# Kernel tuning notes

Measured on AMD Instinct MI355X. Metric: run time of the kernel, lower is better.

Reference implementation:

```python
import jax, jax.numpy as jnp
import numpy as np
from jax import lax

S = 2                      # window half-size (matches init_kwargs s)
K = 2 * S + 1              # kernel size = 5
SZ = float(K ** 3)         # number of voxels in the window
EPS = 1e-10


def _box_sum(x):
    """Replicate-pad then valid 3D box-sum with an all-ones K^3 kernel.
    x: [N, 1, D, H, W] -> [N, 1, D, H, W]. Same math as F.pad(mode='replicate')
    followed by Conv3d(ones kernel, valid)."""
    xp = jnp.pad(x, ((0, 0), (0, 0), (S, S), (S, S), (S, S)), mode='edge')
    kern = jnp.ones((1, 1, K, K, K), dtype=x.dtype)
    return lax.conv_general_dilated(
        xp, kern, window_strides=(1, 1, 1), padding='VALID',
        dimension_numbers=('NCDHW', 'OIDHW', 'NCDHW'))


def setup_inputs() -> dict:
    key = jax.random.key(0)
    k1, k2 = jax.random.split(key)
    shape = (2, 1, 160, 160, 160)
    im_fixed = jax.random.normal(k1, shape, dtype=jnp.float32)
    im_moving = jax.random.normal(k2, shape, dtype=jnp.float32)
    mask = jnp.ones(shape, dtype=jnp.float32)
    return {"im_fixed": im_fixed, "im_moving": im_moving, "mask": mask}


def reference(im_fixed, im_moving, mask):
    # local means
    u_F = _box_sum(im_fixed) / SZ
    u_M = _box_sum(im_moving) / SZ
    # local variances (box-sum of squared centered values, then / SZ)
    sigma_F = jnp.sqrt(_box_sum((im_fixed - u_F) ** 2) / SZ)
    sigma_M = jnp.sqrt(_box_sum((im_moving - u_M) ** 2) / SZ)
    # normalized images
    n_F = (im_fixed - u_F) / (sigma_F + EPS)
    n_M = (im_moving - u_M) / (sigma_M + EPS)
    # local cross-correlation map (box-sum, NOT divided by SZ, as in torch code)
    cross = _box_sum(n_F * n_M)
    # reduce: negative masked sum of squared LCC
    return -1.0 * jnp.sum(cross ** 2 * mask)
```

## Files before the change

### kernel.cpp

```cpp
#include <hip/hip_runtime.h>

namespace {

constexpr int LEN   = 160;
constexpr int PLANE = LEN * LEN;
constexpr int VOL   = LEN * PLANE;
constexpr float INV_SZ = 1.0f / 125.0f;
constexpr float EPS_   = 1e-10f;

constexpr int BLK = 512;

constexpr int FTX = 32, FTY = 16, FZC = 32;
constexpr int FRX = FTX + 4, FRY = FTY + 4;
constexpr int FNRAW = FRX * FRY;
constexpr int FNBX = 5, FNBY = 10, FNXY = 50, FNCHZ = 5;

constexpr int STX = 32, STY = 32, SZC = 16;
constexpr int SRX = STX + 4, SRY = STY + 4;
constexpr int SNRAW = SRX * SRY;
constexpr int SNBX = 5, SNBY = 5, SNXY = 25, SNCHZ = 10;

constexpr int NWG = 500, QW = 62, RW = 4;

__device__ __forceinline__ int clampi(int v) {
  return v < 0 ? 0 : (v > LEN - 1 ? LEN - 1 : v);
}

__device__ __forceinline__ int swz(int g) {
  const int xcd = g & 7, idx = g >> 3;
  return (xcd < RW) ? xcd * (QW + 1) + idx
                    : RW * (QW + 1) + (xcd - RW) * QW + idx;
}

__global__ __launch_bounds__(BLK) void fuseAB(const float* __restrict__ inA,
                                              const float* __restrict__ inB,
                                              float* __restrict__ outP) {
  __shared__ __align__(16) float raw[2][2][FRY][FRX];
  __shared__ __align__(16) float xs [4][2][FRY][FTX];

  const int tid = threadIdx.x;
  const int g = blockIdx.x + FNBX * (blockIdx.y + FNBY * blockIdx.z);
  const int w = swz(g);
  const int batch = w / 250, rem = w % 250;
  const int zc = rem / FNXY, tl = rem % FNXY;
  const int x0 = (tl % FNBX) * FTX;
  const int y0 = (tl / FNBX) * FTY;
  const int z0 = zc * FZC;
  const size_t base = (size_t)batch * VOL;

  int off[2]; float* ldst[2][2][2];
  bool act[2];
#pragma unroll
  for (int j = 0; j < 2; ++j) {
    int i = tid + j * BLK;
    act[j] = i < FNRAW;
    int ii = act[j] ? i : 0;
    const int ry = ii / FRX, rx = ii % FRX;
    off[j] = clampi(y0 - 2 + ry) * LEN + clampi(x0 - 2 + rx);
#pragma unroll
    for (int f = 0; f < 2; ++f)
#pragma unroll
      for (int p = 0; p < 2; ++p) ldst[j][f][p] = &raw[f][p][ry][rx];
  }

  const float* tsrc[2]; float* tdst[2];
#pragma unroll
  for (int k = 0; k < 2; ++k) {
    int tt = (k == 0) ? tid : tid + BLK;
    if (tt >= 640) tt = 0;
    const int p = tt / 320, r1 = tt % 320;
    const int f = r1 / 160, r2 = r1 % 160;
    const int r = r2 / 8,  c = r2 % 8;
    tsrc[k] = &raw[f][p][r][4 * c];
    tdst[k] = &xs[f][p][r][4 * c];
  }

  const bool qact = tid < 256;
  const int ly  = tid >> 4;
  const int lx0 = (tid & 15) * 2;
  const int sOff = (y0 + ly) * LEN + (x0 + lx0);

  float pA[2][2], pB[2][2];
  float2 rzF[6], rzM[6], rzF2[6], rzM2[6];
  float2 cnF[4], cnM[4];

  auto loadPair = [&](int t) {
#pragma unroll
    for (int p = 0; p < 2; ++p) {
      const size_t pb = base + (size_t)clampi(t + p) * PLANE;
#pragma unroll
      for (int j = 0; j < 2; ++j)
        if (act[j]) { pA[p][j] = inA[pb + off[j]]; pB[p][j] = inB[pb + off[j]]; }
    }
  };
  auto depositPair = [&]() {
#pragma unroll
    for (int p = 0; p < 2; ++p)
#pragma unroll
      for (int j = 0; j < 2; ++j)
        if (act[j]) { *ldst[j][0][p] = pA[p][j]; *ldst[j][1][p] = pB[p][j]; }
  };

  auto xsumTask = [&](int k) {
    const float4 u = *(const float4*)tsrc[k];
    const float4 v = *(const float4*)(tsrc[k] + 4);
    const float m = u.y + u.z + u.w;
    float4 s;
    s.x = m + u.x + v.x;
    s.y = m + v.x + v.y;
    s.z = s.y - u.y + v.z;
    s.w = s.z - u.z + v.w;
    *(float4*)tdst[k] = s;
    float4 uq, vq;
    uq.x = u.x * u.x; uq.y = u.y * u.y; uq.z = u.z * u.z; uq.w = u.w * u.w;
    vq.x = v.x * v.x; vq.y = v.y * v.y; vq.z = v.z * v.z; vq.w = v.w * v.w;
    const float mq = uq.y + uq.z + uq.w;
    float4 q;
    q.x = mq + uq.x + vq.x;
    q.y = mq + vq.x + vq.y;
    q.z = q.y - uq.y + vq.z;
    q.w = q.z - uq.z + vq.w;
    *(float4*)(tdst[k] + 2 * 2 * FRY * FTX) = q;
  };

  loadPair(z0 - 2);
  depositPair();
  __syncthreads();

  for (int t = z0 - 2; t <= z0 + FZC; t += 2) {
    if (t + 2 <= z0 + FZC) loadPair(t + 2);

    xsumTask(0);
    if (tid < 128) xsumTask(1);

    if (qact) {
      cnF[0] = cnF[2]; cnF[1] = cnF[3]; cnM[0] = cnM[2]; cnM[1] = cnM[3];
      cnF[2] = *(const float2*)&raw[0][0][ly + 2][lx0 + 2];
      cnF[3] = *(const float2*)&raw[0][1][ly + 2][lx0 + 2];
      cnM[2] = *(const float2*)&raw[1][0][ly + 2][lx0 + 2];
      cnM[3] = *(const float2*)&raw[1][1][ly + 2][lx0 + 2];
    }

    __syncthreads();

    if (t + 2 <= z0 + FZC) depositPair();

    if (qact) {
#pragma unroll
      for (int s = 0; s < 4; ++s) {
        rzF[s] = rzF[s + 2]; rzM[s] = rzM[s + 2];
        rzF2[s] = rzF2[s + 2]; rzM2[s] = rzM2[s + 2];
      }
#pragma unroll
      for (int p = 0; p < 2; ++p) {
        float2 sf = {0.f, 0.f}, sm = {0.f, 0.f};
        float2 sf2 = {0.f, 0.f}, sm2 = {0.f, 0.f};
#pragma unroll
        for (int k = 0; k < 5; ++k) {
          const float2 a  = *(const float2*)&xs[0][p][ly + k][lx0];
          const float2 b  = *(const float2*)&xs[1][p][ly + k][lx0];
          const float2 a2 = *(const float2*)&xs[2][p][ly + k][lx0];
          const float2 b2 = *(const float2*)&xs[3][p][ly + k][lx0];
          sf.x += a.x;   sf.y += a.y;   sm.x += b.x;   sm.y += b.y;
          sf2.x += a2.x; sf2.y += a2.y; sm2.x += b2.x; sm2.y += b2.y;
        }
        rzF[4 + p] = sf; rzM[4 + p] = sm;
        rzF2[4 + p] = sf2; rzM2[4 + p] = sm2;
      }

      if (t >= z0 + 2) {
#pragma unroll
        for (int q = 0; q < 2; ++q) {
          const int zo = t - 2 + q;
          float2 bF = {0.f, 0.f}, bM = {0.f, 0.f};
          float2 bF2 = {0.f, 0.f}, bM2 = {0.f, 0.f};
#pragma unroll
          for (int s = 0; s < 5; ++s) {
            bF.x += rzF[q + s].x;   bF.y += rzF[q + s].y;
            bM.x += rzM[q + s].x;   bM.y += rzM[q + s].y;
            bF2.x += rzF2[q + s].x; bF2.y += rzF2[q + s].y;
            bM2.x += rzM2[q + s].x; bM2.y += rzM2[q + s].y;
          }
          float2 o;
          {
            const float uF = bF.x * INV_SZ, uM = bM.x * INV_SZ;
            const float vF = fmaxf(bF2.x * INV_SZ - uF * uF, 0.f);
            const float vM = fmaxf(bM2.x * INV_SZ - uM * uM, 0.f);
            o.x = ((cnF[q].x - uF) * (cnM[q].x - uM)) /
                  ((sqrtf(vF) + EPS_) * (sqrtf(vM) + EPS_));
          }
          {
            const float uF = bF.y * INV_SZ, uM = bM.y * INV_SZ;
            const float vF = fmaxf(bF2.y * INV_SZ - uF * uF, 0.f);
            const float vM = fmaxf(bM2.y * INV_SZ - uM * uM, 0.f);
            o.y = ((cnF[q].y - uF) * (cnM[q].y - uM)) /
                  ((sqrtf(vF) + EPS_) * (sqrtf(vM) + EPS_));
          }
          *(float2*)&outP[base + (size_t)zo * PLANE + sOff] = o;
        }
      }
    }
    __syncthreads();
  }
}

__global__ __launch_bounds__(BLK) void slab1_reduce(const float* __restrict__ p,
                                                    const float* __restrict__ mask,
                                                    float* __restrict__ out) {
  __shared__ __align__(16) float raw[2][SRY][SRX];
  __shared__ __align__(16) float xs [2][SRY][SRX];
  __shared__ float wsum[BLK / 64];

  const int tid = threadIdx.x;
  const int g = blockIdx.x + SNBX * (blockIdx.y + SNBY * blockIdx.z);
  const int w = swz(g);
  const int batch = w / 250, rem = w % 250;
  const int zc = rem / SNXY, tl = rem % SNXY;
  const int x0 = (tl % SNBX) * STX;
  const int y0 = (tl / SNBX) * STY;
  const int z0 = zc * SZC;
  const size_t base = (size_t)batch * VOL;

  int off[3], lly[3], llx[3];
  bool act[3];
#pragma unroll
  for (int j = 0; j < 3; ++j) {
    int i = tid + j * BLK;
    act[j] = i < SNRAW;
    int ii = act[j] ? i : 0;
    lly[j] = ii / SRX; llx[j] = ii % SRX;
    off[j] = clampi(y0 - 2 + lly[j]) * LEN + clampi(x0 - 2 + llx[j]);
  }
  const int ly  = tid >> 4;
  const int lx0 = (tid & 15) * 2;

  float pf[2][3];
  float2 rz[6];
  float acc = 0.f;

  auto loadPair = [&](int t) {
#pragma unroll
    for (int pp = 0; pp < 2; ++pp) {
      const size_t pb = base + (size_t)clampi(t + pp) * PLANE;
#pragma unroll
      for (int j = 0; j < 3; ++j)
        if (act[j]) pf[pp][j] = p[pb + off[j]];
    }
  };
  auto depositPair = [&]() {
#pragma unroll
    for (int pp = 0; pp < 2; ++pp)
#pragma unroll
      for (int j = 0; j < 3; ++j)
        if (act[j]) raw[pp][lly[j]][llx[j]] = pf[pp][j];
  };

  loadPair(z0 - 2);
  depositPair();
  __syncthreads();

  for (int t = z0 - 2; t <= z0 + SZC; t += 2) {
    if (t + 2 <= z0 + SZC) loadPair(t + 2);

    if (tid < 288) {
      const int c = tid & 7, r = tid >> 3;
#pragma unroll
      for (int pp = 0; pp < 2; ++pp) {
        const float* rp = &raw[pp][r][4 * c];
        const float4 u = *(const float4*)rp;
        const float4 v = *(const float4*)(rp + 4);
        const float m = u.y + u.z + u.w;
        float4 s;
        s.x = m + u.x + v.x;
        s.y = m + v.x + v.y;
        s.z = s.y - u.y + v.z;
        s.w = s.z - u.z + v.w;
        *(float4*)&xs[pp][r][4 * c] = s;
      }
    }
    __syncthreads();

    if (t + 2 <= z0 + SZC) depositPair();

#pragma unroll
    for (int s = 0; s < 4; ++s) rz[s] = rz[s + 2];
#pragma unroll
    for (int pp = 0; pp < 2; ++pp) {
      float2 s2 = {0.f, 0.f};
#pragma unroll
      for (int k = 0; k < 5; ++k) {
        const float2 a = *(const float2*)&xs[pp][ly + k][lx0];
        s2.x += a.x; s2.y += a.y;
      }
      rz[4 + pp] = s2;
    }

    if (t >= z0 + 2) {
#pragma unroll
      for (int q = 0; q < 2; ++q) {
        const int zo = t - 2 + q;
        float2 bs = {0.f, 0.f};
#pragma unroll
        for (int s = 0; s < 5; ++s) { bs.x += rz[q + s].x; bs.y += rz[q + s].y; }
        const size_t gg = base + (size_t)zo * PLANE + (size_t)(y0 + ly) * LEN + (x0 + lx0);
        const float2 mk = *(const float2*)&mask[gg];
        acc += bs.x * bs.x * mk.x + bs.y * bs.y * mk.y;
      }
    }
    __syncthreads();
  }

#pragma unroll
  for (int o = 32; o > 0; o >>= 1) acc += __shfl_down(acc, o, 64);
  const int lane = tid & 63, wid = tid >> 6;
  if (lane == 0) wsum[wid] = acc;
  __syncthreads();
  if (tid == 0) {
    float tt = 0.f;
#pragma unroll
    for (int ww = 0; ww < BLK / 64; ++ww) tt += wsum[ww];
    atomicAdd(out, -tt);
  }
}

}

extern "C" void kernel_launch(void* const* d_in, const int* in_sizes, int n_in,
                              void* d_out, int out_size, void* d_ws, size_t ws_size,
                              hipStream_t stream) {
  const float* F    = (const float*)d_in[0];
  const float* M    = (const float*)d_in[1];
  const float* mask = (const float*)d_in[2];
  float* out = (float*)d_out;

  float* pB = (float*)d_ws;

  hipMemsetAsync(d_out, 0, sizeof(float), stream);

  dim3 gf(FNBX, FNBY, FNCHZ * 2), blk(BLK);
  dim3 gs(SNBX, SNBY, SNCHZ * 2);

  fuseAB<<<gf, blk, 0, stream>>>(F, M, pB);
  slab1_reduce<<<gs, blk, 0, stream>>>(pB, mask, out);
}
```

Before: 163.3 us.

## Double-buffer LDS slabs and deepen global prefetch in both stencil kernels

Both kernels now keep two LDS copies of the raw and x-summed slabs and alternate between them. Each z-step needs one barrier instead of two, and global loads are issued two steps ahead into a second register set. The aim is to hide barrier and global-load latency on the streaming z-loop. In exchange LDS use per block roughly doubles, to about 63 KB in fuseAB, and register pressure rises, which may lower the number of resident blocks.

Result: no change. 162.8 us (-0.3%).

```diff
diff --git a/kernel.cpp b/kernel.cpp
--- a/kernel.cpp
+++ b/kernel.cpp
@@ -20,7 +20,7 @@
 constexpr int SNRAW = SRX * SRY;
 constexpr int SNBX = 5, SNBY = 5, SNXY = 25, SNCHZ = 10;
 
-constexpr int NWG = 500, QW = 62, RW = 4;
+constexpr int QW = 62, RW = 4;
 
 __device__ __forceinline__ int clampi(int v) {
   return v < 0 ? 0 : (v > LEN - 1 ? LEN - 1 : v);
@@ -35,8 +35,12 @@
 __global__ __launch_bounds__(BLK) void fuseAB(const float* __restrict__ inA,
                                               const float* __restrict__ inB,
                                               float* __restrict__ outP) {
-  __shared__ __align__(16) float raw[2][2][FRY][FRX];
-  __shared__ __align__(16) float xs [4][2][FRY][FTX];
+  __shared__ __align__(16) float raw[2][2][2][FRY][FRX];
+  __shared__ __align__(16) float xs [2][4][2][FRY][FTX];
+  constexpr int RAWB = 2 * 2 * FRY * FRX;
+  constexpr int XSB  = 4 * 2 * FRY * FTX;
+  constexpr int AS   = 2 * FRY * FTX;
+  constexpr int PS   = FRY * FTX;
 
   const int tid = threadIdx.x;
   const int g = blockIdx.x + FNBX * (blockIdx.y + FNBY * blockIdx.z);
@@ -48,7 +52,7 @@
   const int z0 = zc * FZC;
   const size_t base = (size_t)batch * VOL;
 
-  int off[2]; float* ldst[2][2][2];
+  int off[2]; float* ld0[2][2][2];
   bool act[2];
 #pragma unroll
   for (int j = 0; j < 2; ++j) {
@@ -60,10 +64,10 @@
 #pragma unroll
     for (int f = 0; f < 2; ++f)
 #pragma unroll
-      for (int p = 0; p < 2; ++p) ldst[j][f][p] = &raw[f][p][ry][rx];
-  }
-
-  const float* tsrc[2]; float* tdst[2];
+      for (int p = 0; p < 2; ++p) ld0[j][f][p] = &raw[0][f][p][ry][rx];
+  }
+
+  const float* ts0[2]; float* td0[2];
 #pragma unroll
   for (int k = 0; k < 2; ++k) {
     int tt = (k == 0) ? tid : tid + BLK;
@@ -71,46 +75,52 @@
     const int p = tt / 320, r1 = tt % 320;
     const int f = r1 / 160, r2 = r1 % 160;
     const int r = r2 / 8,  c = r2 % 8;
-    tsrc[k] = &raw[f][p][r][4 * c];
-    tdst[k] = &xs[f][p][r][4 * c];
+    ts0[k] = &raw[0][f][p][r][4 * c];
+    td0[k] = &xs[0][f][p][r][4 * c];
   }
 
   const bool qact = tid < 256;
   const int ly  = tid >> 4;
   const int lx0 = (tid & 15) * 2;
   const int sOff = (y0 + ly) * LEN + (x0 + lx0);
-
-  float pA[2][2], pB[2][2];
+  const float* yb0 = &xs[0][0][0][ly][lx0];
+
+  float s0A[2][2], s0B[2][2], s1A[2][2], s1B[2][2];
   float2 rzF[6], rzM[6], rzF2[6], rzM2[6];
   float2 cnF[4], cnM[4];
 
-  auto loadPair = [&](int t) {
+  auto loadPair = [&](int t, float (&ra)[2][2], float (&rb)[2][2]) {
 #pragma unroll
     for (int p = 0; p < 2; ++p) {
       const size_t pb = base + (size_t)clampi(t + p) * PLANE;
 #pragma unroll
       for (int j = 0; j < 2; ++j)
-        if (act[j]) { pA[p][j] = inA[pb + off[j]]; pB[p][j] = inB[pb + off[j]]; }
-    }
-  };
-  auto depositPair = [&]() {
+        if (act[j]) { ra[p][j] = inA[pb + off[j]]; rb[p][j] = inB[pb + off[j]]; }
+    }
+  };
+  auto depositPair = [&](int buf, float (&ra)[2][2], float (&rb)[2][2]) {
 #pragma unroll
     for (int p = 0; p < 2; ++p)
 #pragma unroll
       for (int j = 0; j < 2; ++j)
-        if (act[j]) { *ldst[j][0][p] = pA[p][j]; *ldst[j][1][p] = pB[p][j]; }
-  };
-
-  auto xsumTask = [&](int k) {
-    const float4 u = *(const float4*)tsrc[k];
-    const float4 v = *(const float4*)(tsrc[k] + 4);
+        if (act[j]) {
+          ld0[j][0][p][buf * RAWB] = ra[p][j];
+          ld0[j][1][p][buf * RAWB] = rb[p][j];
+        }
+  };
+
+  auto xsumTask = [&](int buf, int k) {
+    const float* src = ts0[k] + buf * RAWB;
+    float* dst = td0[k] + buf * XSB;
+    const float4 u = *(const float4*)src;
+    const float4 v = *(const float4*)(src + 4);
     const float m = u.y + u.z + u.w;
     float4 s;
     s.x = m + u.x + v.x;
     s.y = m + v.x + v.y;
     s.z = s.y - u.y + v.z;
     s.w = s.z - u.z + v.w;
-    *(float4*)tdst[k] = s;
+    *(float4*)dst = s;
     float4 uq, vq;
     uq.x = u.x * u.x; uq.y = u.y * u.y; uq.z = u.z * u.z; uq.w = u.w * u.w;
     vq.x = v.x * v.x; vq.y = v.y * v.y; vq.z = v.z * v.z; vq.w = v.w * v.w;
@@ -120,30 +130,27 @@
     q.y = mq + vq.x + vq.y;
     q.z = q.y - uq.y + vq.z;
     q.w = q.z - uq.z + vq.w;
-    *(float4*)(tdst[k] + 2 * 2 * FRY * FTX) = q;
-  };
-
-  loadPair(z0 - 2);
-  depositPair();
-  __syncthreads();
-
-  for (int t = z0 - 2; t <= z0 + FZC; t += 2) {
-    if (t + 2 <= z0 + FZC) loadPair(t + 2);
-
-    xsumTask(0);
-    if (tid < 128) xsumTask(1);
+    *(float4*)(dst + 2 * AS) = q;
+  };
+
+  auto body = [&](int buf, int t,
+                  float (&dA)[2][2], float (&dB)[2][2],
+                  float (&lA)[2][2], float (&lB)[2][2]) {
+    if (t + 2 <= z0 + FZC) depositPair(buf ^ 1, dA, dB);
+    if (t + 4 <= z0 + FZC) loadPair(t + 4, lA, lB);
+
+    xsumTask(buf, 0);
+    if (tid < 128) xsumTask(buf, 1);
 
     if (qact) {
       cnF[0] = cnF[2]; cnF[1] = cnF[3]; cnM[0] = cnM[2]; cnM[1] = cnM[3];
-      cnF[2] = *(const float2*)&raw[0][0][ly + 2][lx0 + 2];
-      cnF[3] = *(const float2*)&raw[0][1][ly + 2][lx0 + 2];
-      cnM[2] = *(const float2*)&raw[1][0][ly + 2][lx0 + 2];
-      cnM[3] = *(const float2*)&raw[1][1][ly + 2][lx0 + 2];
+      cnF[2] = *(const float2*)&raw[buf][0][0][ly + 2][lx0 + 2];
+      cnF[3] = *(const float2*)&raw[buf][0][1][ly + 2][lx0 + 2];
+      cnM[2] = *(const float2*)&raw[buf][1][0][ly + 2][lx0 + 2];
+      cnM[3] = *(const float2*)&raw[buf][1][1][ly + 2][lx0 + 2];
     }
 
     __syncthreads();
-
-    if (t + 2 <= z0 + FZC) depositPair();
 
     if (qact) {
 #pragma unroll
@@ -151,16 +158,17 @@
         rzF[s] = rzF[s + 2]; rzM[s] = rzM[s + 2];
         rzF2[s] = rzF2[s + 2]; rzM2[s] = rzM2[s + 2];
       }
+      const float* yb = yb0 + buf * XSB;
 #pragma unroll
       for (int p = 0; p < 2; ++p) {
         float2 sf = {0.f, 0.f}, sm = {0.f, 0.f};
         float2 sf2 = {0.f, 0.f}, sm2 = {0.f, 0.f};
 #pragma unroll
         for (int k = 0; k < 5; ++k) {
-          const float2 a  = *(const float2*)&xs[0][p][ly + k][lx0];
-          const float2 b  = *(const float2*)&xs[1][p][ly + k][lx0];
-          const float2 a2 = *(const float2*)&xs[2][p][ly + k][lx0];
-          const float2 b2 = *(const float2*)&xs[3][p][ly + k][lx0];
+          const float2 a  = *(const float2*)(yb + 0 * AS + p * PS + k * FTX);
+          const float2 b  = *(const float2*)(yb + 1 * AS + p * PS + k * FTX);
+          const float2 a2 = *(const float2*)(yb + 2 * AS + p * PS + k * FTX);
+          const float2 b2 = *(const float2*)(yb + 3 * AS + p * PS + k * FTX);
           sf.x += a.x;   sf.y += a.y;   sm.x += b.x;   sm.y += b.y;
           sf2.x += a2.x; sf2.y += a2.y; sm2.x += b2.x; sm2.y += b2.y;
         }
@@ -200,16 +208,26 @@
         }
       }
     }
-    __syncthreads();
+  };
+
+  loadPair(z0 - 2, s0A, s0B);
+  depositPair(0, s0A, s0B);
+  loadPair(z0, s1A, s1B);
+  __syncthreads();
+
+  for (int t = z0 - 2; t <= z0 + FZC; t += 4) {
+    body(0, t,     s1A, s1B, s0A, s0B);
+    body(1, t + 2, s0A, s0B, s1A, s1B);
   }
 }
 
 __global__ __launch_bounds__(BLK) void slab1_reduce(const float* __restrict__ p,
                                                     const float* __restrict__ mask,
                                                     float* __restrict__ out) {
-  __shared__ __align__(16) float raw[2][SRY][SRX];
-  __shared__ __align__(16) float xs [2][SRY][SRX];
+  __shared__ __align__(16) float raw[2][2][SRY][SRX];
+  __shared__ __align__(16) float xs [2][2][SRY][SRX];
   __shared__ float wsum[BLK / 64];
+  constexpr int RAWB = 2 * SRY * SRX;
 
   const int tid = threadIdx.x;
   const int g = blockIdx.x + SNBX * (blockIdx.y + SNBY * blockIdx.z);
@@ -221,52 +239,51 @@
   const int z0 = zc * SZC;
   const size_t base = (size_t)batch * VOL;
 
-  int off[3], lly[3], llx[3];
+  int off[3]; float* ld0[3][2];
   bool act[3];
 #pragma unroll
   for (int j = 0; j < 3; ++j) {
     int i = tid + j * BLK;
     act[j] = i < SNRAW;
     int ii = act[j] ? i : 0;
-    lly[j] = ii / SRX; llx[j] = ii % SRX;
-    off[j] = clampi(y0 - 2 + lly[j]) * LEN + clampi(x0 - 2 + llx[j]);
+    const int ry = ii / SRX, rx = ii % SRX;
+    off[j] = clampi(y0 - 2 + ry) * LEN + clampi(x0 - 2 + rx);
+#pragma unroll
+    for (int pp = 0; pp < 2; ++pp) ld0[j][pp] = &raw[0][pp][ry][rx];
   }
   const int ly  = tid >> 4;
   const int lx0 = (tid & 15) * 2;
 
-  float pf[2][3];
+  float s0[2][3], s1[2][3];
   float2 rz[6];
   float acc = 0.f;
 
-  auto loadPair = [&](int t) {
+  auto loadPair = [&](int t, float (&r)[2][3]) {
 #pragma unroll
     for (int pp = 0; pp < 2; ++pp) {
       const size_t pb = base + (size_t)clampi(t + pp) * PLANE;
 #pragma unroll
       for (int j = 0; j < 3; ++j)
-        if (act[j]) pf[pp][j] = p[pb + off[j]];
-    }
-  };
-  auto depositPair = [&]() {
+        if (act[j]) r[pp][j] = p[pb + off[j]];
+    }
+  };
+  auto depositPair = [&](int buf, float (&r)[2][3]) {
 #pragma unroll
     for (int pp = 0; pp < 2; ++pp)
 #pragma unroll
       for (int j = 0; j < 3; ++j)
-        if (act[j]) raw[pp][lly[j]][llx[j]] = pf[pp][j];
-  };
-
-  loadPair(z0 - 2);
-  depositPair();
-  __syncthreads();
-
-  for (int t = z0 - 2; t <= z0 + SZC; t += 2) {
-    if (t + 2 <= z0 + SZC) loadPair(t + 2);
+        if (act[j]) ld0[j][pp][buf * RAWB] = r[pp][j];
+  };
+
+  auto body = [&](int buf, int t, float (&dep)[2][3], float (&ld)[2][3]) {
+    if (t + 2 <= z0 + SZC) depositPair(buf ^ 1, dep);
+    if (t + 4 <= z0 + SZC) loadPair(t + 4, ld);
 
     if (tid < 288) {
       const int c = tid & 7, r = tid >> 3;
 #pragma unroll
       for (int pp = 0; pp < 2; ++pp) {
-        const float* rp = &raw[pp][r][4 * c];
+        const float* rp = &raw[buf][pp][r][4 * c];
         const float4 u = *(const float4*)rp;
         const float4 v = *(const float4*)(rp + 4);
         const float m = u.y + u.z + u.w;
@@ -275,12 +292,11 @@
         s.y = m + v.x + v.y;
         s.z = s.y - u.y + v.z;
         s.w = s.z - u.z + v.w;
-        *(float4*)&xs[pp][r][4 * c] = s;
-      }
-    }
+        *(float4*)&xs[buf][pp][r][4 * c] = s;
+      }
+    }
+
     __syncthreads();
-
-    if (t + 2 <= z0 + SZC) depositPair();
 
 #pragma unroll
     for (int s = 0; s < 4; ++s) rz[s] = rz[s + 2];
@@ -289,7 +305,7 @@
       float2 s2 = {0.f, 0.f};
 #pragma unroll
       for (int k = 0; k < 5; ++k) {
-        const float2 a = *(const float2*)&xs[pp][ly + k][lx0];
+        const float2 a = *(const float2*)&xs[buf][pp][ly + k][lx0];
         s2.x += a.x; s2.y += a.y;
       }
       rz[4 + pp] = s2;
@@ -302,12 +318,22 @@
         float2 bs = {0.f, 0.f};
 #pragma unroll
         for (int s = 0; s < 5; ++s) { bs.x += rz[q + s].x; bs.y += rz[q + s].y; }
-        const size_t gg = base + (size_t)zo * PLANE + (size_t)(y0 + ly) * LEN + (x0 + lx0);
+        const size_t gg = base + (size_t)zo * PLANE +
+                          (size_t)(y0 + ly) * LEN + (x0 + lx0);
         const float2 mk = *(const float2*)&mask[gg];
         acc += bs.x * bs.x * mk.x + bs.y * bs.y * mk.y;
       }
     }
-    __syncthreads();
+  };
+
+  loadPair(z0 - 2, s0);
+  depositPair(0, s0);
+  loadPair(z0, s1);
+  __syncthreads();
+
+  for (int t = z0 - 2; t <= z0 + SZC; t += 4) {
+    body(0, t,     s1, s0);
+    body(1, t + 2, s0, s1);
   }
 
 #pragma unroll
```
